# Kernel tuning notes

Hardware: AMD Instinct MI355X
Metric: run time of the kernel (lower is better)

Reference implementation:

```python
import jax, jax.numpy as jnp
import numpy as np

# ProbAttention (Yangskm/DroneMA-i-), eval mode (dropout=identity).
# Key facts from the source: mask_flag=False, scale=None -> `if self.scale` is
# False, so scores are NOT divided by sqrt(D). The _prob_QK sampling/topk result
# `u` and _get_initial_context are dead code w.r.t. the returned context, so the
# output is exactly dense softmax attention. Inputs are (B, L, H, D); the module
# transposes to (B, H, L, D) and transposes back at the end.

def setup_inputs() -> dict:
    key = jax.random.key(0)
    k1, k2, k3 = jax.random.split(key, 3)
    B, L, H, D = 4, 2048, 8, 64
    return {
        "queries": jax.random.normal(k1, (B, L, H, D), dtype=jnp.float32),
        "keys": jax.random.normal(k2, (B, L, H, D), dtype=jnp.float32),
        "values": jax.random.normal(k3, (B, L, H, D), dtype=jnp.float32),
    }

def reference(queries, keys, values):
    # (B, L, H, D) -> (B, H, L, D)
    q = jnp.swapaxes(queries, 1, 2)
    k = jnp.swapaxes(keys, 1, 2)
    v = jnp.swapaxes(values, 1, 2)
    # dense scores, NO 1/sqrt(D) scaling (scale=None in the original)
    scores = jnp.einsum("bhqd,bhkd->bhqk", q, k)
    attn = jax.nn.softmax(scores, axis=-1)
    ctx = jnp.einsum("bhqk,bhkd->bhqd", attn, v)
    # back to (B, L, H, D)
    return jnp.swapaxes(ctx, 1, 2)
```

## Files before the change

kernel.cpp:

```cpp
#include <hip/hip_runtime.h>
#include <hip/hip_bf16.h>


#define B_ 4
#define L_ 2048
#define H_ 8
#define D_ 64
#define RST_ 512
#define QW_ 32
#define QB_ 128
#define KT_ 64
#define NT_ (L_ / KT_)
#define RS_ 88
#define PS_ 40
#define OTS_ 68
#define SCW_ 35
#define LOG2E_ 1.44269504088896f

#define SMEM_BYTES 35840

typedef _Float16 f16x8 __attribute__((ext_vector_type(8)));
typedef __bf16   bf16x8 __attribute__((ext_vector_type(8)));
typedef float    f32x4 __attribute__((ext_vector_type(4)));

__device__ __forceinline__ unsigned pk_bf16(float a, float b) {
    const __bf16 x = (__bf16)a, y = (__bf16)b;
    return ((unsigned)__builtin_bit_cast(unsigned short, y) << 16) |
           (unsigned)__builtin_bit_cast(unsigned short, x);
}

__global__ __launch_bounds__(512, 4) void attn_ksplit(
    const float* __restrict__ Qg, const float* __restrict__ Kg,
    const float* __restrict__ Vg, float* __restrict__ Og)
{
    __shared__ __align__(16) char smem[SMEM_BYTES];
    _Float16* Kf = (_Float16*)smem;
    __bf16*   Vt = (__bf16*)(smem + 11264);
    __bf16*   Pl = (__bf16*)(smem + 22528);
    float*    Sc = (float*)smem;

    const int tid  = threadIdx.x;
    const int w    = tid >> 6;
    const int qsub = w & 3;
    const int ks   = w >> 2;
    const int ln   = tid & 15;
    const int lg   = (tid >> 4) & 3;

    const int blk   = (blockIdx.x & 7) * 64 + (blockIdx.x >> 3);
    const int qtile = blk & (L_ / QB_ - 1);
    const int bh    = blk >> 4;
    const int h     = bh & (H_ - 1);
    const int b     = bh >> 3;

    const size_t bhbase = (size_t)b * (L_ * H_ * D_) + (size_t)h * D_;
    const int    qbase  = qtile * QB_ + qsub * QW_;

    f16x8 qf[2][2];
#pragma unroll
    for (int ms = 0; ms < 2; ++ms) {
#pragma unroll
        for (int dc = 0; dc < 2; ++dc) {
            const float* src = Qg + bhbase
                + (size_t)(qbase + ms * 16 + ln) * RST_ + dc * 32 + lg * 8;
            const float4 a = ((const float4*)src)[0];
            const float4 c = ((const float4*)src)[1];
            f16x8 f;
            f[0] = (_Float16)(a.x * LOG2E_); f[1] = (_Float16)(a.y * LOG2E_);
            f[2] = (_Float16)(a.z * LOG2E_); f[3] = (_Float16)(a.w * LOG2E_);
            f[4] = (_Float16)(c.x * LOG2E_); f[5] = (_Float16)(c.y * LOG2E_);
            f[6] = (_Float16)(c.z * LOG2E_); f[7] = (_Float16)(c.w * LOG2E_);
            qf[ms][dc] = f;
        }
    }

    f32x4 o[2][4];
    f32x4 lsum[2];
#pragma unroll
    for (int ms = 0; ms < 2; ++ms) {
        lsum[ms] = (f32x4){0.f, 0.f, 0.f, 0.f};
#pragma unroll
        for (int dg = 0; dg < 4; ++dg) o[ms][dg] = (f32x4){0.f, 0.f, 0.f, 0.f};
    }

    bf16x8 onesb;
#pragma unroll
    for (int j = 0; j < 8; ++j) onesb[j] = (__bf16)1.0f;

    const int krow = tid >> 3;
    const int kd8  = (tid & 7) * 8;
    const int vkp  = (tid & 31) * 2;
    const int vdb  = (tid >> 5) * 4;
    const float* kbase = Kg + bhbase;
    const float* vbase = Vg + bhbase;

    float4 kr0, kr1, vr0, vr1;

    auto issue = [&](int kt) {
        const float* ksrc = kbase + (size_t)(kt + krow) * RST_ + kd8;
        kr0 = ((const float4*)ksrc)[0];
        kr1 = ((const float4*)ksrc)[1];
        const float* vsrc = vbase + (size_t)(kt + vkp) * RST_ + vdb;
        vr0 = ((const float4*)vsrc)[0];
        vr1 = ((const float4*)(vsrc + RST_))[0];
    };
    auto writeKV = [&]() {
        f16x8 kw;
        kw[0] = (_Float16)kr0.x; kw[1] = (_Float16)kr0.y;
        kw[2] = (_Float16)kr0.z; kw[3] = (_Float16)kr0.w;
        kw[4] = (_Float16)kr1.x; kw[5] = (_Float16)kr1.y;
        kw[6] = (_Float16)kr1.z; kw[7] = (_Float16)kr1.w;
        *(f16x8*)&Kf[krow * RS_ + kd8] = kw;
        const float av[4] = {vr0.x, vr0.y, vr0.z, vr0.w};
        const float bv[4] = {vr1.x, vr1.y, vr1.z, vr1.w};
#pragma unroll
        for (int i = 0; i < 4; ++i)
            *(unsigned*)&Vt[(vdb + i) * RS_ + vkp] = pk_bf16(av[i], bv[i]);
    };

    __bf16* Pw = &Pl[(w * 16) * PS_];

    auto compute = [&]() {
        f16x8 kfr[2][2];
#pragma unroll
        for (int dc = 0; dc < 2; ++dc)
#pragma unroll
            for (int kg = 0; kg < 2; ++kg)
                kfr[dc][kg] = *(const f16x8*)
                    &Kf[(ks * 32 + kg * 16 + ln) * RS_ + dc * 32 + lg * 8];

#pragma unroll
        for (int ms = 0; ms < 2; ++ms) {
            f32x4 st[2];
#pragma unroll
            for (int kg = 0; kg < 2; ++kg) st[kg] = (f32x4){0.f, 0.f, 0.f, 0.f};
#pragma unroll
            for (int dc = 0; dc < 2; ++dc)
#pragma unroll
                for (int kg = 0; kg < 2; ++kg)
                    st[kg] = __builtin_amdgcn_mfma_f32_16x16x32_f16(
                        kfr[dc][kg], qf[ms][dc], st[kg], 0, 0, 0);

#pragma unroll
            for (int kg = 0; kg < 2; ++kg) {
                const float p0 = __builtin_amdgcn_exp2f(st[kg][0]);
                const float p1 = __builtin_amdgcn_exp2f(st[kg][1]);
                const float p2 = __builtin_amdgcn_exp2f(st[kg][2]);
                const float p3 = __builtin_amdgcn_exp2f(st[kg][3]);
                const unsigned long long u =
                    (unsigned long long)pk_bf16(p0, p1) |
                    ((unsigned long long)pk_bf16(p2, p3) << 32);
                *(unsigned long long*)&Pw[ln * PS_ + kg * 16 + lg * 4] = u;
            }
            const bf16x8 pf = *(const bf16x8*)&Pw[ln * PS_ + lg * 8];

            lsum[ms] = __builtin_amdgcn_mfma_f32_16x16x32_bf16(onesb, pf, lsum[ms], 0, 0, 0);
#pragma unroll
            for (int dg = 0; dg < 4; ++dg) {
                const bf16x8 vfd = *(const bf16x8*)
                    &Vt[(dg * 16 + ln) * RS_ + ks * 32 + lg * 8];
                o[ms][dg] = __builtin_amdgcn_mfma_f32_16x16x32_bf16(vfd, pf, o[ms][dg], 0, 0, 0);
            }
        }
    };

    issue(0);
    for (int t = 0; t < NT_; ++t) {
        __syncthreads();
        writeKV();
        __syncthreads();
        if (t + 1 < NT_) issue((t + 1) * KT_);
        compute();
    }

    const int lane = tid & 63;
    __syncthreads();
    if (w >= 4) {
        float* sc = &Sc[((w - 4) * 64 + lane) * SCW_];
#pragma unroll
        for (int ms = 0; ms < 2; ++ms)
#pragma unroll
            for (int dg = 0; dg < 4; ++dg)
#pragma unroll
                for (int r = 0; r < 4; ++r)
                    sc[ms * 16 + dg * 4 + r] = o[ms][dg][r];
        sc[32] = lsum[0][0];
        sc[33] = lsum[1][0];
    }
    __syncthreads();
    if (w < 4) {
        const float* sc = &Sc[(w * 64 + lane) * SCW_];
        float po[2][4][4];
#pragma unroll
        for (int ms = 0; ms < 2; ++ms)
#pragma unroll
            for (int dg = 0; dg < 4; ++dg)
#pragma unroll
                for (int r = 0; r < 4; ++r)
                    po[ms][dg][r] = o[ms][dg][r] + sc[ms * 16 + dg * 4 + r];
        const float linv[2] = {1.0f / (lsum[0][0] + sc[32]),
                               1.0f / (lsum[1][0] + sc[33])};

        float* Ot = (float*)(smem + w * 8960);
        const int qr = lane >> 2;
        const int ch = lane & 3;
#pragma unroll
        for (int ms = 0; ms < 2; ++ms) {
#pragma unroll
            for (int dg = 0; dg < 4; ++dg) {
#pragma unroll
                for (int i = 0; i < 2; ++i) {
                    float2 pr;
                    pr.x = po[ms][dg][2 * i]     * linv[ms];
                    pr.y = po[ms][dg][2 * i + 1] * linv[ms];
                    *(float2*)&Ot[ln * OTS_ + dg * 16 + lg * 4 + 2 * i] = pr;
                }
            }
#pragma unroll
            for (int p = 0; p < 4; ++p) {
                const float4 vo = *(const float4*)&Ot[qr * OTS_ + ch * 4 + p * 16];
                *(float4*)(Og + bhbase
                    + (size_t)(qbase + ms * 16 + qr) * RST_ + ch * 4 + p * 16) = vo;
            }
        }
    }
}

extern "C" void kernel_launch(void* const* d_in, const int* in_sizes, int n_in,
                              void* d_out, int out_size, void* d_ws, size_t ws_size,
                              hipStream_t stream) {
    const float* Q = (const float*)d_in[0];
    const float* K = (const float*)d_in[1];
    const float* V = (const float*)d_in[2];
    float* O = (float*)d_out;

    const int grid = B_ * H_ * (L_ / QB_);
    attn_ksplit<<<grid, 512, 0, stream>>>(Q, K, V, O);
}
```

Baseline: 70.44 us.

## Feed softmax P directly from registers via 16x16x16 bf16 MFMA, drop LDS round-trip

Replaces the P shuffle through LDS (write then reload as bf16x8) with the 16x16x16 bf16 MFMA variant. Its operand layout matches the score accumulator layout, so the exp'd probabilities go straight from registers into the PV and row-sum MFMAs. V fragments are preloaded per tile, s_setprio hints wrap the MFMA groups, and the K/V pointers are advanced incrementally. This removes LDS traffic and waits on the P path, at the cost of twice as many (smaller) MFMA instructions for PV and lsum and more registers held for V.

New measurement: 64.20 us. -8.8%, faster.

```diff
diff --git a/kernel.cpp b/kernel.cpp
--- a/kernel.cpp
+++ b/kernel.cpp
@@ -12,7 +12,6 @@
 #define KT_ 64
 #define NT_ (L_ / KT_)
 #define RS_ 88
-#define PS_ 40
 #define OTS_ 68
 #define SCW_ 35
 #define LOG2E_ 1.44269504088896f
@@ -20,7 +19,7 @@
 #define SMEM_BYTES 35840
 
 typedef _Float16 f16x8 __attribute__((ext_vector_type(8)));
-typedef __bf16   bf16x8 __attribute__((ext_vector_type(8)));
+typedef short    s16x4 __attribute__((ext_vector_type(4)));
 typedef float    f32x4 __attribute__((ext_vector_type(4)));
 
 __device__ __forceinline__ unsigned pk_bf16(float a, float b) {
@@ -29,14 +28,17 @@
            (unsigned)__builtin_bit_cast(unsigned short, x);
 }
 
-__global__ __launch_bounds__(512, 4) void attn_ksplit(
+__device__ __forceinline__ f32x4 mfma16_bf16(s16x4 a, s16x4 b, f32x4 c) {
+    return __builtin_amdgcn_mfma_f32_16x16x16bf16_1k(a, b, c, 0, 0, 0);
+}
+
+__global__ __launch_bounds__(512, 4) void attn_k16pv(
     const float* __restrict__ Qg, const float* __restrict__ Kg,
     const float* __restrict__ Vg, float* __restrict__ Og)
 {
     __shared__ __align__(16) char smem[SMEM_BYTES];
     _Float16* Kf = (_Float16*)smem;
     __bf16*   Vt = (__bf16*)(smem + 11264);
-    __bf16*   Pl = (__bf16*)(smem + 22528);
     float*    Sc = (float*)smem;
 
     const int tid  = threadIdx.x;
@@ -82,26 +84,30 @@
         for (int dg = 0; dg < 4; ++dg) o[ms][dg] = (f32x4){0.f, 0.f, 0.f, 0.f};
     }
 
-    bf16x8 onesb;
-#pragma unroll
-    for (int j = 0; j < 8; ++j) onesb[j] = (__bf16)1.0f;
+    s16x4 ones4;
+#pragma unroll
+    for (int j = 0; j < 4; ++j) ones4[j] = (short)0x3F80;
 
     const int krow = tid >> 3;
     const int kd8  = (tid & 7) * 8;
     const int vkp  = (tid & 31) * 2;
     const int vdb  = (tid >> 5) * 4;
-    const float* kbase = Kg + bhbase;
-    const float* vbase = Vg + bhbase;
-
-    float4 kr0, kr1, vr0, vr1;
-
-    auto issue = [&](int kt) {
-        const float* ksrc = kbase + (size_t)(kt + krow) * RST_ + kd8;
-        kr0 = ((const float4*)ksrc)[0];
-        kr1 = ((const float4*)ksrc)[1];
-        const float* vsrc = vbase + (size_t)(kt + vkp) * RST_ + vdb;
-        vr0 = ((const float4*)vsrc)[0];
-        vr1 = ((const float4*)(vsrc + RST_))[0];
+
+    const float* kp  = Kg + bhbase + (size_t)krow * RST_ + kd8;
+    const float* vp  = Vg + bhbase + (size_t)vkp * RST_ + vdb;
+
+    float4 kr0, kr1;
+    float  vr0[4], vr1[4];
+
+    auto issue = [&]() {
+        kr0 = ((const float4*)kp)[0];
+        kr1 = ((const float4*)kp)[1];
+        const float4 a = ((const float4*)vp)[0];
+        const float4 c = ((const float4*)(vp + RST_))[0];
+        vr0[0] = a.x; vr0[1] = a.y; vr0[2] = a.z; vr0[3] = a.w;
+        vr1[0] = c.x; vr1[1] = c.y; vr1[2] = c.z; vr1[3] = c.w;
+        kp += KT_ * RST_;
+        vp += KT_ * RST_;
     };
     auto writeKV = [&]() {
         f16x8 kw;
@@ -110,14 +116,10 @@
         kw[4] = (_Float16)kr1.x; kw[5] = (_Float16)kr1.y;
         kw[6] = (_Float16)kr1.z; kw[7] = (_Float16)kr1.w;
         *(f16x8*)&Kf[krow * RS_ + kd8] = kw;
-        const float av[4] = {vr0.x, vr0.y, vr0.z, vr0.w};
-        const float bv[4] = {vr1.x, vr1.y, vr1.z, vr1.w};
 #pragma unroll
         for (int i = 0; i < 4; ++i)
-            *(unsigned*)&Vt[(vdb + i) * RS_ + vkp] = pk_bf16(av[i], bv[i]);
+            *(unsigned*)&Vt[(vdb + i) * RS_ + vkp] = pk_bf16(vr0[i], vr1[i]);
     };
-
-    __bf16* Pw = &Pl[(w * 16) * PS_];
 
     auto compute = [&]() {
         f16x8 kfr[2][2];
@@ -127,48 +129,59 @@
             for (int kg = 0; kg < 2; ++kg)
                 kfr[dc][kg] = *(const f16x8*)
                     &Kf[(ks * 32 + kg * 16 + ln) * RS_ + dc * 32 + lg * 8];
+        s16x4 vf[2][4];
+#pragma unroll
+        for (int kg = 0; kg < 2; ++kg)
+#pragma unroll
+            for (int dg = 0; dg < 4; ++dg)
+                vf[kg][dg] = *(const s16x4*)
+                    &Vt[(dg * 16 + ln) * RS_ + ks * 32 + kg * 16 + lg * 4];
 
 #pragma unroll
         for (int ms = 0; ms < 2; ++ms) {
             f32x4 st[2];
 #pragma unroll
             for (int kg = 0; kg < 2; ++kg) st[kg] = (f32x4){0.f, 0.f, 0.f, 0.f};
+            __builtin_amdgcn_s_setprio(1);
 #pragma unroll
             for (int dc = 0; dc < 2; ++dc)
 #pragma unroll
                 for (int kg = 0; kg < 2; ++kg)
                     st[kg] = __builtin_amdgcn_mfma_f32_16x16x32_f16(
                         kfr[dc][kg], qf[ms][dc], st[kg], 0, 0, 0);
-
+            __builtin_amdgcn_s_setprio(0);
+
+            s16x4 pf[2];
 #pragma unroll
             for (int kg = 0; kg < 2; ++kg) {
                 const float p0 = __builtin_amdgcn_exp2f(st[kg][0]);
                 const float p1 = __builtin_amdgcn_exp2f(st[kg][1]);
                 const float p2 = __builtin_amdgcn_exp2f(st[kg][2]);
                 const float p3 = __builtin_amdgcn_exp2f(st[kg][3]);
-                const unsigned long long u =
-                    (unsigned long long)pk_bf16(p0, p1) |
-                    ((unsigned long long)pk_bf16(p2, p3) << 32);
-                *(unsigned long long*)&Pw[ln * PS_ + kg * 16 + lg * 4] = u;
-            }
-            const bf16x8 pf = *(const bf16x8*)&Pw[ln * PS_ + lg * 8];
-
-            lsum[ms] = __builtin_amdgcn_mfma_f32_16x16x32_bf16(onesb, pf, lsum[ms], 0, 0, 0);
-#pragma unroll
-            for (int dg = 0; dg < 4; ++dg) {
-                const bf16x8 vfd = *(const bf16x8*)
-                    &Vt[(dg * 16 + ln) * RS_ + ks * 32 + lg * 8];
-                o[ms][dg] = __builtin_amdgcn_mfma_f32_16x16x32_bf16(vfd, pf, o[ms][dg], 0, 0, 0);
-            }
+                union { unsigned u[2]; s16x4 v; } pu;
+                pu.u[0] = pk_bf16(p0, p1);
+                pu.u[1] = pk_bf16(p2, p3);
+                pf[kg] = pu.v;
+            }
+
+            __builtin_amdgcn_s_setprio(1);
+#pragma unroll
+            for (int kg = 0; kg < 2; ++kg) {
+                lsum[ms] = mfma16_bf16(ones4, pf[kg], lsum[ms]);
+#pragma unroll
+                for (int dg = 0; dg < 4; ++dg)
+                    o[ms][dg] = mfma16_bf16(vf[kg][dg], pf[kg], o[ms][dg]);
+            }
+            __builtin_amdgcn_s_setprio(0);
         }
     };
 
-    issue(0);
+    issue();
     for (int t = 0; t < NT_; ++t) {
         __syncthreads();
         writeKV();
         __syncthreads();
-        if (t + 1 < NT_) issue((t + 1) * KT_);
+        if (t + 1 < NT_) issue();
         compute();
     }
 
@@ -234,5 +247,5 @@
     float* O = (float*)d_out;
 
     const int grid = B_ * H_ * (L_ / QB_);
-    attn_ksplit<<<grid, 512, 0, stream>>>(Q, K, V, O);
-}
+    attn_k16pv<<<grid, 512, 0, stream>>>(Q, K, V, O);
+}
```
